# Kernel optimization log

Hardware: AMD Instinct MI355X
Metric: run time of the kernel (lower is better)

The kernel has to match this reference:

```python
import jax, jax.numpy as jnp
import numpy as np

B, K, N = 8192, 10, 100
LAM = 1.0


def _vec_transpose_P():
    # 9x9 vec-transpose permutation: P[3i+j, 3j+i] = 1 (the _getP matrix)
    P = np.zeros((9, 9), dtype=np.float32)
    for i in range(3):
        for j in range(3):
            P[3 * i + j, 3 * j + i] = 1.0
    return jnp.asarray(P)


def setup_inputs() -> dict:
    key = jax.random.key(0)
    k1, k2, k3 = jax.random.split(key, 3)
    weights = jax.random.uniform(k1, (N, 1), dtype=jnp.float32) + 0.1  # positive weights
    model_keypoints = jax.random.normal(k2, (K, 3, N), dtype=jnp.float32)
    y = jax.random.normal(k3, (B, 3, N), dtype=jnp.float32)
    return {"y": y, "weights": weights, "model_keypoints": model_keypoints}


def _pace_forward(y, weights, model_keypoints):
    n = model_keypoints.shape[-1]
    k = model_keypoints.shape[0]
    bsz = y.shape[0]
    w = weights                                  # (N,1)
    wsum = w.sum()
    b = model_keypoints                          # (K,3,N)
    b_w = (b @ w) / wsum                         # (K,3,1)
    sw = jnp.sqrt(w[:, 0])                       # (N,)

    # ---- precomputed constants (original __init__) ----
    bar_b = sw[None, None, :] * (b - b_w)                    # (K,3,N)
    bar_B = bar_b.transpose(0, 2, 1).reshape(k, 3 * n).T     # (3N,K), row idx 3n+a
    bar_H = 2.0 * (bar_B.T @ bar_B + LAM * jnp.eye(k, dtype=y.dtype))
    Hinv = jnp.linalg.inv(bar_H)
    Ht = Hinv @ jnp.ones((k, 1), dtype=y.dtype)
    denom = Ht.sum()
    G = Hinv - (Ht @ Ht.T) / denom               # (K,K)
    g = Ht / denom                               # (K,1)
    GBt = G @ bar_B.T                            # (K,3N)
    M = jnp.concatenate([2.0 * bar_B @ GBt - jnp.eye(3 * n, dtype=y.dtype),
                         2.0 * jnp.sqrt(LAM) * GBt], axis=0)       # (3N+K,3N)
    h = jnp.concatenate([bar_B @ g, jnp.sqrt(LAM) * g], axis=0)    # (3N+K,1)
    P = _vec_transpose_P().astype(y.dtype)

    # ---- forward ----
    y_w = (y @ w) / wsum                         # (B,3,1)
    bar_y = sw[None, None, :] * (y - y_w)        # (B,3,N)

    # E_b = M @ kron(Ybar_b^T, I3) @ P, done batched without materializing kron:
    # (M @ kron(Y^T, I3))[m, 3j+a] = sum_n M[m, 3n+a] * Y[j, n]
    Mr = M.reshape(-1, n, 3)                                  # Mr[m, nn, a] = M[m, 3nn+a]
    MB = jnp.einsum('mna,bjn->bmja', Mr, bar_y)               # (B,3N+K,3,3)
    E = MB.reshape(bsz, -1, 9) @ P                            # (B,3N+K,9)
    q00 = h[:, 0] @ h[:, 0]                                   # scalar h^T h
    hE = jnp.einsum('m,bmc->bc', h[:, 0], E)                  # (B,9)
    Q11 = jnp.einsum('bmc,bmd->bcd', E, E)                    # (B,9,9)
    top = jnp.concatenate([jnp.broadcast_to(q00, (bsz, 1, 1)), hE[:, None, :]], axis=2)
    bot = jnp.concatenate([hE[:, :, None], Q11], axis=2)
    Q = jnp.concatenate([top, bot], axis=1)                   # (B,10,10)

    # SDP relaxation: at a tight optimum X = v v^T with v the minimizer of v^T Q v,
    # recovered here as the eigenvector of Q with smallest eigenvalue (batched eigh)
    _, evec = jnp.linalg.eigh(Q)
    v = evec[:, :, 0]                                         # (B,10), ascending order
    v = v / v[:, :1]                                          # homogenize: v[0] = 1
    R = v[:, 1:].reshape(bsz, 3, 3).transpose(0, 2, 1)        # (B,3,3)

    # shape coefficients: c = 2 * G B^T * kron(I_N, R^T) vec(bar_y) + g
    RTy = jnp.einsum('bra,brn->bna', R, bar_y).reshape(bsz, 3 * n)   # idx 3n+a
    c = 2.0 * jnp.einsum('km,bm->bk', GBt, RTy)[:, :, None] + g[None, :, :]  # (B,K,1)
    # translation: t = y_w - R b_w^T c
    t = y_w - R @ jnp.einsum('ka,bko->bao', b_w[:, :, 0], c)  # (B,3,1)
    return R, t, c


def reference(y, weights, model_keypoints):
    return _pace_forward(y, weights, model_keypoints)
```

## Files before the change

kernel.cpp:

```cpp
#include <hip/hip_runtime.h>
#include <math.h>

#define LT_CT 0
#define LT_WT 3200
#define LT_SM 3304
#define LT_AR 3600
#define LT_TOT 11184

#define SM_WSUM 0
#define SM_RWS  1
#define SM_Q00  2
#define SM_Z2   4
#define SM_BS   16
#define SM_W    48
#define SM_G    148
#define SM_GV   248
#define SM_BW   260

#define A_YS 0
#define A_SF 4864
#define A_QL 6416
#define A_AX 7328

__host__ __device__ constexpr int TRI(int p,int q){ return p*10-(p*(p+1))/2+q; }
__host__ __device__ constexpr int SIDX(int a,int b){ return (a<=b)?TRI(a,b):TRI(b,a); }
__host__ __device__ constexpr int LTRI(int i,int j){ return i*(i+1)/2+j; }

template<int CTRL>
__device__ __forceinline__ float dpp_add(float v){
  int s = __builtin_amdgcn_mov_dpp(__float_as_int(v), CTRL, 0xF, 0xF, true);
  return v + __int_as_float(s);
}
__device__ __forceinline__ float gsum16(float v){
  v = dpp_add<0xB1>(v);
  v = dpp_add<0x4E>(v);
  v = dpp_add<0x141>(v);
  v = dpp_add<0x140>(v);
  return v;
}

__global__ __launch_bounds__(256,2) void pace_fused(const float* __restrict__ y,
                                                    const float* __restrict__ w,
                                                    const float* __restrict__ mk,
                                                    float* __restrict__ out){
  __shared__ __attribute__((aligned(16))) float S[LT_TOT];
  const int tid  = threadIdx.x;
  const int lane = tid & 63;
  const int sub  = tid & 15;
  const int item = tid >> 4;

  {
    float* s_mb = S+LT_AR;
    float* s_w  = S+LT_AR+3000;
    float* s_sw = S+LT_AR+3104;
    float* s_bw = S+LT_AR+3208;
    float* s_C  = S+LT_AR+3240;
    float* s_Hi = S+LT_AR+3340;
    float* s_G  = S+LT_AR+3440;
    float* s_T  = S+LT_AR+3540;
    float* s_gv = S+LT_AR+3640;
    float* s_Ht = S+LT_AR+3652;
    float* s_z  = S+LT_AR+3664;
    float* sm   = S+LT_SM;

    for (int i=tid;i<3000;i+=256) s_mb[i]=mk[i];
    for (int i=tid;i<100;i+=256){ float x=w[i]; s_w[i]=x; s_sw[i]=sqrtf(x); }
    __syncthreads();

    float av = s_w[lane] + ((lane<36)? s_w[lane+64] : 0.f);
    #pragma unroll
    for (int m=32;m;m>>=1) av += __shfl_xor(av,m);
    const float wsum = av;
    const float rws  = 1.0f/av;

    if (tid<30){
      const float4* p=(const float4*)&s_mb[tid*100];
      const float4* q=(const float4*)&s_w[0];
      float acc=0;
      #pragma unroll 5
      for (int j=0;j<25;j++){ float4 x=p[j], yv=q[j];
        acc=fmaf(x.x,yv.x,acc); acc=fmaf(x.y,yv.y,acc);
        acc=fmaf(x.z,yv.z,acc); acc=fmaf(x.w,yv.w,acc); }
      s_bw[tid]=acc*rws;
    }
    __syncthreads();
    for (int i=tid;i<3000;i+=256){ int r=i/100, n=i-r*100; s_mb[i]=s_sw[n]*(s_mb[i]-s_bw[r]); }
    __syncthreads();
    if (tid<100){
      int k=tid/10, k2=tid-10*(tid/10);
      const float4* p1=(const float4*)&s_mb[k*300];
      const float4* p2=(const float4*)&s_mb[k2*300];
      float acc=0;
      #pragma unroll 5
      for (int j=0;j<75;j++){ float4 x=p1[j], yv=p2[j];
        acc=fmaf(x.x,yv.x,acc); acc=fmaf(x.y,yv.y,acc);
        acc=fmaf(x.z,yv.z,acc); acc=fmaf(x.w,yv.w,acc); }
      s_C[tid]=acc;
    }
    __syncthreads();
    if (tid<64){
      float R[20];
      {
        int row=(tid<10)? tid : 0;
        #pragma unroll
        for (int c=0;c<10;c++) R[c]=2.0f*(s_C[row*10+c]+(c==row?1.0f:0.0f));
        #pragma unroll
        for (int c=0;c<10;c++) R[10+c]=(c==row)?1.0f:0.0f;
      }
      #pragma unroll
      for (int p=0;p<10;p++){
        float appv=__shfl(R[p],p);
        float ra=1.0f/appv;
        float fr=R[p];
        #pragma unroll
        for (int c=0;c<20;c++){
          float pc=__shfl(R[c],p)*ra;
          R[c]=(tid==p)? pc : fmaf(-fr,pc,R[c]);
        }
      }
      if (tid<10){
        float ht=0.f;
        #pragma unroll
        for (int c=0;c<10;c++){ s_Hi[tid*10+c]=R[10+c]; ht+=R[10+c]; }
        s_Ht[tid]=ht;
      }
    }
    __syncthreads();
    float dsum=0.f;
    #pragma unroll
    for (int k=0;k<10;k++) dsum+=s_Ht[k];
    const float rden=1.0f/dsum;
    if (tid<10) s_gv[tid]=s_Ht[tid]*rden;
    __syncthreads();
    if (tid<100){ int r=tid/10,c=tid-10*(tid/10); s_G[tid]=s_Hi[tid]-s_Ht[r]*s_Ht[c]*rden; }
    __syncthreads();
    if (tid<100){
      int r=tid/10,c=tid-10*(tid/10); float acc=0;
      #pragma unroll
      for (int j=0;j<10;j++) acc+=(s_C[r*10+j]+(r==j?1.0f:0.0f))*s_G[j*10+c];
      s_T[tid]=acc;
    }
    __syncthreads();
    if (tid<100){
      int r=tid/10,c=tid-10*(tid/10); float acc=0;
      #pragma unroll
      for (int j=0;j<10;j++) acc+=s_G[r*10+j]*s_T[j*10+c];
      sm[SM_W+tid]=4.0f*acc-4.0f*s_G[tid];
      sm[SM_G+tid]=s_G[tid];
    }
    if (tid<10){
      float acc=0;
      #pragma unroll
      for (int j=0;j<10;j++) acc+=(s_C[tid*10+j]+(tid==j?1.0f:0.0f))*s_gv[j];
      s_z[tid]=acc;
    }
    __syncthreads();
    if (tid<10){
      float acc=0;
      #pragma unroll
      for (int j=0;j<10;j++) acc+=s_G[tid*10+j]*s_z[j];
      sm[SM_Z2+tid]=2.0f*acc-s_gv[tid];
    }
    if (tid==0){
      float acc=0;
      #pragma unroll
      for (int r=0;r<10;r++){
        float rr=0;
        #pragma unroll
        for (int c=0;c<10;c++) rr+=s_C[r*10+c]*s_gv[c];
        acc+=s_gv[r]*rr+s_gv[r]*s_gv[r];
      }
      sm[SM_WSUM]=wsum; sm[SM_RWS]=rws; sm[SM_Q00]=acc; sm[3]=0.f;
    }
    for (int i=tid;i<3000;i+=256){
      int l=i/100, n=i-100*l;
      S[LT_CT + ((n>>2)*32 + l)*4 + (n&3)] = s_mb[i]*s_sw[n];
    }
    for (int i=tid;i<200;i+=256){ int c=i>>3, r=i&7; S[LT_CT+(c*32+30)*4+r]=0.f; }
    for (int i=tid;i<100;i+=256) S[LT_WT+i]=s_w[i];
    if (tid<30){
      const float4* p=(const float4*)&s_mb[tid*100];
      const float4* q=(const float4*)&s_sw[0];
      float acc=0;
      #pragma unroll 5
      for (int j=0;j<25;j++){ float4 x=p[j], yv=q[j];
        acc=fmaf(x.x,yv.x,acc); acc=fmaf(x.y,yv.y,acc);
        acc=fmaf(x.z,yv.z,acc); acc=fmaf(x.w,yv.w,acc); }
      sm[SM_BS+tid]=acc;
    }
    if (tid<2)  sm[SM_BS+30+tid]=0.f;
    if (tid<10) sm[SM_GV+tid]=s_gv[tid];
    if (tid<30) sm[SM_BW+tid]=s_bw[tid];
    __syncthreads();
  }

  const float* sm = S+LT_SM;
  float* yS = S+LT_AR+A_YS;
  float* sF = S+LT_AR+A_SF;
  float* sQ = S+LT_AR+A_QL;
  float* sX = S+LT_AR+A_AX;

  {
    const float4* yg = (const float4*)(y + (size_t)blockIdx.x*4800);
    #pragma unroll
    for (int r=0;r<5;r++){
      int f = tid + 256*r;
      if (f<1200){
        int it2=f/75, rem=f-75*it2;
        ((float4*)&yS[it2*304])[rem] = yg[f];
      }
    }
  }
  __syncthreads();

  const float* yb = &yS[item*304];

  float swy0=0,swy1=0,swy2=0,s00=0,s01=0,s02=0,s11=0,s12=0,s22=0;
  #pragma unroll
  for (int m=0;m<6;m++){
    int n=sub+16*m;
    float y0=yb[n], y1=yb[100+n], y2=yb[200+n];
    float wn=S[LT_WT+n];
    float wy0=wn*y0,wy1=wn*y1,wy2=wn*y2;
    swy0+=wy0;swy1+=wy1;swy2+=wy2;
    s00+=wy0*y0;s01+=wy0*y1;s02+=wy0*y2;s11+=wy1*y1;s12+=wy1*y2;s22+=wy2*y2;
  }
  if (sub<4){
    int n=96+sub;
    float y0=yb[n], y1=yb[100+n], y2=yb[200+n];
    float wn=S[LT_WT+n];
    float wy0=wn*y0,wy1=wn*y1,wy2=wn*y2;
    swy0+=wy0;swy1+=wy1;swy2+=wy2;
    s00+=wy0*y0;s01+=wy0*y1;s02+=wy0*y2;s11+=wy1*y1;s12+=wy1*y2;s22+=wy2*y2;
  }
  swy0=gsum16(swy0); swy1=gsum16(swy1); swy2=gsum16(swy2);
  s00=gsum16(s00); s01=gsum16(s01); s02=gsum16(s02);
  s11=gsum16(s11); s12=gsum16(s12); s22=gsum16(s22);

  const float wsum=sm[SM_WSUM], rws=sm[SM_RWS];
  const float yw0=swy0*rws, yw1=swy1*rws, yw2=swy2*rws;

  {
    float a0=0,a1=0,a2=0,b0=0,b1=0,b2=0;
    #pragma unroll 5
    for (int c=0;c<25;c++){
      float4 cfA = *(const float4*)&S[LT_CT+(c*32+sub)*4];
      float4 cfB = *(const float4*)&S[LT_CT+(c*32+sub+16)*4];
      float4 ya  = *(const float4*)&yb[4*c];
      float4 yB  = *(const float4*)&yb[100+4*c];
      float4 yc  = *(const float4*)&yb[200+4*c];
      a0=fmaf(cfA.x,ya.x,a0); a0=fmaf(cfA.y,ya.y,a0); a0=fmaf(cfA.z,ya.z,a0); a0=fmaf(cfA.w,ya.w,a0);
      a1=fmaf(cfA.x,yB.x,a1); a1=fmaf(cfA.y,yB.y,a1); a1=fmaf(cfA.z,yB.z,a1); a1=fmaf(cfA.w,yB.w,a1);
      a2=fmaf(cfA.x,yc.x,a2); a2=fmaf(cfA.y,yc.y,a2); a2=fmaf(cfA.z,yc.z,a2); a2=fmaf(cfA.w,yc.w,a2);
      b0=fmaf(cfB.x,ya.x,b0); b0=fmaf(cfB.y,ya.y,b0); b0=fmaf(cfB.z,ya.z,b0); b0=fmaf(cfB.w,ya.w,b0);
      b1=fmaf(cfB.x,yB.x,b1); b1=fmaf(cfB.y,yB.y,b1); b1=fmaf(cfB.z,yB.z,b1); b1=fmaf(cfB.w,yB.w,b1);
      b2=fmaf(cfB.x,yc.x,b2); b2=fmaf(cfB.y,yc.y,b2); b2=fmaf(cfB.z,yc.z,b2); b2=fmaf(cfB.w,yc.w,b2);
    }
    float bsA=sm[SM_BS+sub], bsB=sm[SM_BS+sub+16];
    a0-=yw0*bsA; a1-=yw1*bsA; a2-=yw2*bsA;
    b0-=yw0*bsB; b1-=yw1*bsB; b2-=yw2*bsB;
    sF[item*97+sub*3+0]=a0; sF[item*97+sub*3+1]=a1; sF[item*97+sub*3+2]=a2;
    sF[item*97+48+sub*3+0]=b0; sF[item*97+48+sub*3+1]=b1; sF[item*97+48+sub*3+2]=b2;
    if (sub==0){
      float* ax=&sX[item*16];
      ax[0]=yw0; ax[1]=yw1; ax[2]=yw2;
      ax[3+0]=s00-wsum*yw0*yw0;
      ax[3+4]=s11-wsum*yw1*yw1;
      ax[3+8]=s22-wsum*yw2*yw2;
      float g01=s01-wsum*yw0*yw1, g02=s02-wsum*yw0*yw2, g12=s12-wsum*yw1*yw2;
      ax[3+1]=g01; ax[3+3]=g01;
      ax[3+2]=g02; ax[3+6]=g02;
      ax[3+5]=g12; ax[3+7]=g12;
    }
  }
  __syncthreads();

  if (tid<144){
    int it2=tid/9, mp=tid-9*(tid/9);
    float fcol[10], t2[10];
    #pragma unroll
    for (int k=0;k<10;k++) fcol[k]=sF[it2*97+k*9+mp];
    #pragma unroll
    for (int k=0;k<10;k++){
      float acc=0;
      #pragma unroll
      for (int k2=0;k2<10;k2++) acc+=sm[SM_W+k*10+k2]*fcol[k2];
      t2[k]=acc;
    }
    float he=0;
    #pragma unroll
    for (int k=0;k<10;k++) he+=sm[SM_Z2+k]*fcol[k];
    sQ[it2*57 + 1+mp]=he;
    #pragma unroll 1
    for (int m=0;m<=mp;m++){
      float gd=sX[it2*16+3+(m%3)*3+(mp%3)];
      float acc=((m/3)==(mp/3))? gd : 0.f;
      #pragma unroll
      for (int k=0;k<10;k++) acc+=sF[it2*97+k*9+m]*t2[k];
      int p=1+m, q=1+mp;
      sQ[it2*57 + p*10-((p*(p+1))>>1)+q]=acc;
    }
  }
  if (tid>=144 && tid<160) sQ[(tid-144)*57]=sm[SM_Q00];
  __syncthreads();

  if (tid<16){
    const int it2=tid;
    const int gb2=blockIdx.x*16+it2;
    float A[55];
    #pragma unroll
    for (int e=0;e<55;e++) A[e]=sQ[it2*57+e];
    float dd[10], ee[9];
    #pragma unroll
    for (int k=0;k<8;k++){
      float nrm2=0.f;
      #pragma unroll
      for (int i=1;i<10;i++){ if (i<k+1) continue; float xi=A[SIDX(i,k)]; nrm2=fmaf(xi,xi,nrm2); }
      float x0=A[SIDX(k+1,k)];
      float nr=sqrtf(nrm2);
      float alpha=-copysignf(nr,x0);
      bool ok=nrm2>1e-30f;
      float v1=x0-alpha;
      float vtv=-2.0f*alpha*v1;
      float bh=ok?2.0f*__builtin_amdgcn_rcpf(vtv):0.f;
      ee[k]=ok?alpha:x0;
      float vv[10];
      #pragma unroll
      for (int i=0;i<10;i++) vv[i]=(i<k+1)?0.f:((i==k+1)?v1:A[SIDX(i,k)]);
      float p[10];
      #pragma unroll
      for (int i=0;i<10;i++){
        if (i<k+1){ p[i]=0.f; continue; }
        float acc=0;
        #pragma unroll
        for (int j=1;j<10;j++){ if (j<k+1) continue; acc+=A[SIDX(i,j)]*vv[j]; }
        p[i]=bh*acc;
      }
      float Kc=0.f;
      #pragma unroll
      for (int i=1;i<10;i++){ if (i<k+1) continue; Kc=fmaf(vv[i],p[i],Kc); }
      Kc*=0.5f*bh;
      float wv[10];
      #pragma unroll
      for (int i=0;i<10;i++) wv[i]=p[i]-Kc*vv[i];
      #pragma unroll
      for (int i=1;i<10;i++){
        if (i<k+1) continue;
        #pragma unroll
        for (int j=1;j<10;j++){
          if (j<i) continue;
          A[TRI(i,j)]-=vv[i]*wv[j]+wv[i]*vv[j];
        }
      }
    }
    ee[8]=A[TRI(8,9)];
    #pragma unroll
    for (int i=0;i<10;i++) dd[i]=A[TRI(i,i)];
    float esq[9];
    #pragma unroll
    for (int i=0;i<9;i++) esq[i]=ee[i]*ee[i];

    float scaleT=0.f, lo=1e30f, hi=1e30f;
    #pragma unroll
    for (int i=0;i<10;i++){
      float r=((i>0)?fabsf(ee[i-1]):0.f)+((i<9)?fabsf(ee[i]):0.f);
      scaleT=fmaxf(scaleT,fabsf(dd[i])+r);
      lo=fminf(lo,dd[i]-r);
      hi=fminf(hi,dd[i]);
    }
    hi+=1e-6f*scaleT+1e-30f;
    const float pm=1e-12f*scaleT+1e-37f;
    #pragma unroll 1
    for (int it=0;it<16;++it){
      float mid=0.5f*(lo+hi);
      float q=dd[0]-mid;
      q=(fabsf(q)<pm)?((q<0.f)?-pm:pm):q;
      int cnt=(q<0.f);
      #pragma unroll
      for (int i=1;i<10;i++){
        q=dd[i]-mid-esq[i-1]*__builtin_amdgcn_rcpf(q);
        q=(fabsf(q)<pm)?((q<0.f)?-pm:pm):q;
        cnt+=(q<0.f);
      }
      bool any=cnt>0;
      hi=any?mid:hi;
      lo=any?lo:mid;
    }
    const float sigma=lo-1e-5f*scaleT-1e-30f;
    const float pmL=1e-8f*scaleT+1e-37f;

    float Lc[55], rd[10];
    #pragma unroll
    for (int i=0;i<10;i++){
      #pragma unroll
      for (int j=0;j<10;j++){
        if (j>i) continue;
        float a=sQ[it2*57+SIDX(j,i)]-((i==j)?sigma:0.f);
        #pragma unroll
        for (int t2=0;t2<9;t2++){
          if (t2>=j) continue;
          a-=Lc[LTRI(i,t2)]*Lc[LTRI(j,t2)];
        }
        if (j<i) Lc[LTRI(i,j)]=a*rd[j];
        else { a=fmaxf(a,pmL); rd[i]=rsqrtf(a); Lc[LTRI(i,i)]=a*rd[i]; }
      }
    }
    float xv[10];
    #pragma unroll
    for (int i=0;i<10;i++) xv[i]=1.f;
    #pragma unroll 1
    for (int itr=0;itr<3;++itr){
      #pragma unroll
      for (int i=0;i<10;i++){
        float acc=xv[i];
        #pragma unroll
        for (int j=0;j<9;j++){ if (j>=i) continue; acc-=Lc[LTRI(i,j)]*xv[j]; }
        acc*=rd[i];
        xv[i]=fminf(fmaxf(acc,-1e15f),1e15f);
      }
      #pragma unroll
      for (int i=9;i>=0;i--){
        float acc=xv[i];
        #pragma unroll
        for (int j=9;j>0;j--){ if (j<=i) continue; acc-=Lc[LTRI(j,i)]*xv[j]; }
        acc*=rd[i];
        xv[i]=fminf(fmaxf(acc,-1e15f),1e15f);
      }
      float nn=0.f;
      #pragma unroll
      for (int i=0;i<10;i++) nn=fmaf(xv[i],xv[i],nn);
      nn=fmaxf(nn,1e-30f);
      float sc2=rsqrtf(nn);
      #pragma unroll
      for (int i=0;i<10;i++) xv[i]*=sc2;
    }
    float r0=1.0f/xv[0];
    float vn[10];
    vn[0]=1.f;
    #pragma unroll
    for (int m=1;m<10;m++) vn[m]=xv[m]*r0;

    float dv[10];
    #pragma unroll
    for (int k=0;k<10;k++){
      float acc=0;
      #pragma unroll
      for (int m=0;m<9;m++) acc+=vn[1+m]*sF[it2*97+k*9+m];
      dv[k]=acc;
    }
    float cv[10];
    #pragma unroll
    for (int k=0;k<10;k++){
      float acc=0;
      #pragma unroll
      for (int k2=0;k2<10;k2++) acc+=sm[SM_G+k*10+k2]*dv[k2];
      cv[k]=2.0f*acc+sm[SM_GV+k];
    }
    float e0=0,e1=0,e2=0;
    #pragma unroll
    for (int k=0;k<10;k++){
      e0+=sm[SM_BW+k*3+0]*cv[k];
      e1+=sm[SM_BW+k*3+1]*cv[k];
      e2+=sm[SM_BW+k*3+2]*cv[k];
    }
    float ywa=sX[it2*16+0], ywb=sX[it2*16+1], ywc=sX[it2*16+2];
    #pragma unroll
    for (int i=0;i<3;i++)
      #pragma unroll
      for (int j=0;j<3;j++)
        out[gb2*9+i*3+j]=vn[1+3*j+i];
    out[73728+gb2*3+0]=ywa-(vn[1]*e0+vn[4]*e1+vn[7]*e2);
    out[73728+gb2*3+1]=ywb-(vn[2]*e0+vn[5]*e1+vn[8]*e2);
    out[73728+gb2*3+2]=ywc-(vn[3]*e0+vn[6]*e1+vn[9]*e2);
    #pragma unroll
    for (int k=0;k<10;k++)
      out[98304+gb2*10+k]=cv[k];
  }
}

extern "C" void kernel_launch(void* const* d_in, const int* in_sizes, int n_in,
                              void* d_out, int out_size, void* d_ws, size_t ws_size,
                              hipStream_t stream) {
  const float* y  = (const float*)d_in[0];
  const float* w  = (const float*)d_in[1];
  const float* mk = (const float*)d_in[2];
  float* out = (float*)d_out;
  pace_fused<<<512, 256, 0, stream>>>(y, w, mk, out);
}
```

Baseline: 101.2 us.

## Halve items per block, use 32 lanes per item, double grid size

Each block now handles 8 batch items instead of 16, and 32 threads cooperate per item instead of 16. Each thread now computes one projection column group, where before it computed two. Reductions extend to 32 lanes with an extra ds_swizzle step. The smaller shared-memory footprint allows launch bounds of 4 blocks per CU, and the grid doubles to 1024 blocks. In exchange, every block still recomputes the full per-block constant setup (the K×K inverse and related precomputation), so that redundant prologue work doubles, and fewer threads are active in the eigen stage per block.

After: 112.8 us. 1.12x slower.

```diff
diff --git a/kernel.cpp b/kernel.cpp
--- a/kernel.cpp
+++ b/kernel.cpp
@@ -5,7 +5,7 @@
 #define LT_WT 3200
 #define LT_SM 3304
 #define LT_AR 3600
-#define LT_TOT 11184
+#define LT_TOT 7392
 
 #define SM_WSUM 0
 #define SM_RWS  1
@@ -18,9 +18,9 @@
 #define SM_BW   260
 
 #define A_YS 0
-#define A_SF 4864
-#define A_QL 6416
-#define A_AX 7328
+#define A_SF 2432
+#define A_QL 3208
+#define A_AX 3664
 
 __host__ __device__ constexpr int TRI(int p,int q){ return p*10-(p*(p+1))/2+q; }
 __host__ __device__ constexpr int SIDX(int a,int b){ return (a<=b)?TRI(a,b):TRI(b,a); }
@@ -31,23 +31,24 @@
   int s = __builtin_amdgcn_mov_dpp(__float_as_int(v), CTRL, 0xF, 0xF, true);
   return v + __int_as_float(s);
 }
-__device__ __forceinline__ float gsum16(float v){
+__device__ __forceinline__ float gsum32(float v){
   v = dpp_add<0xB1>(v);
   v = dpp_add<0x4E>(v);
   v = dpp_add<0x141>(v);
   v = dpp_add<0x140>(v);
+  v += __int_as_float(__builtin_amdgcn_ds_swizzle(__float_as_int(v), 0x401F));
   return v;
 }
 
-__global__ __launch_bounds__(256,2) void pace_fused(const float* __restrict__ y,
+__global__ __launch_bounds__(256,4) void pace_fused(const float* __restrict__ y,
                                                     const float* __restrict__ w,
                                                     const float* __restrict__ mk,
                                                     float* __restrict__ out){
   __shared__ __attribute__((aligned(16))) float S[LT_TOT];
   const int tid  = threadIdx.x;
   const int lane = tid & 63;
-  const int sub  = tid & 15;
-  const int item = tid >> 4;
+  const int sub  = tid & 31;
+  const int item = tid >> 5;
 
   {
     float* s_mb = S+LT_AR;
@@ -201,11 +202,11 @@
   float* sX = S+LT_AR+A_AX;
 
   {
-    const float4* yg = (const float4*)(y + (size_t)blockIdx.x*4800);
-    #pragma unroll
-    for (int r=0;r<5;r++){
+    const float4* yg = (const float4*)(y + (size_t)blockIdx.x*2400);
+    #pragma unroll
+    for (int r=0;r<3;r++){
       int f = tid + 256*r;
-      if (f<1200){
+      if (f<600){
         int it2=f/75, rem=f-75*it2;
         ((float4*)&yS[it2*304])[rem] = yg[f];
       }
@@ -217,8 +218,8 @@
 
   float swy0=0,swy1=0,swy2=0,s00=0,s01=0,s02=0,s11=0,s12=0,s22=0;
   #pragma unroll
-  for (int m=0;m<6;m++){
-    int n=sub+16*m;
+  for (int m=0;m<3;m++){
+    int n=sub+32*m;
     float y0=yb[n], y1=yb[100+n], y2=yb[200+n];
     float wn=S[LT_WT+n];
     float wy0=wn*y0,wy1=wn*y1,wy2=wn*y2;
@@ -233,34 +234,30 @@
     swy0+=wy0;swy1+=wy1;swy2+=wy2;
     s00+=wy0*y0;s01+=wy0*y1;s02+=wy0*y2;s11+=wy1*y1;s12+=wy1*y2;s22+=wy2*y2;
   }
-  swy0=gsum16(swy0); swy1=gsum16(swy1); swy2=gsum16(swy2);
-  s00=gsum16(s00); s01=gsum16(s01); s02=gsum16(s02);
-  s11=gsum16(s11); s12=gsum16(s12); s22=gsum16(s22);
+  swy0=gsum32(swy0); swy1=gsum32(swy1); swy2=gsum32(swy2);
+  s00=gsum32(s00); s01=gsum32(s01); s02=gsum32(s02);
+  s11=gsum32(s11); s12=gsum32(s12); s22=gsum32(s22);
 
   const float wsum=sm[SM_WSUM], rws=sm[SM_RWS];
   const float yw0=swy0*rws, yw1=swy1*rws, yw2=swy2*rws;
 
   {
-    float a0=0,a1=0,a2=0,b0=0,b1=0,b2=0;
+    float a0=0,a1=0,a2=0;
     #pragma unroll 5
     for (int c=0;c<25;c++){
-      float4 cfA = *(const float4*)&S[LT_CT+(c*32+sub)*4];
-      float4 cfB = *(const float4*)&S[LT_CT+(c*32+sub+16)*4];
-      float4 ya  = *(const float4*)&yb[4*c];
-      float4 yB  = *(const float4*)&yb[100+4*c];
-      float4 yc  = *(const float4*)&yb[200+4*c];
-      a0=fmaf(cfA.x,ya.x,a0); a0=fmaf(cfA.y,ya.y,a0); a0=fmaf(cfA.z,ya.z,a0); a0=fmaf(cfA.w,ya.w,a0);
-      a1=fmaf(cfA.x,yB.x,a1); a1=fmaf(cfA.y,yB.y,a1); a1=fmaf(cfA.z,yB.z,a1); a1=fmaf(cfA.w,yB.w,a1);
-      a2=fmaf(cfA.x,yc.x,a2); a2=fmaf(cfA.y,yc.y,a2); a2=fmaf(cfA.z,yc.z,a2); a2=fmaf(cfA.w,yc.w,a2);
-      b0=fmaf(cfB.x,ya.x,b0); b0=fmaf(cfB.y,ya.y,b0); b0=fmaf(cfB.z,ya.z,b0); b0=fmaf(cfB.w,ya.w,b0);
-      b1=fmaf(cfB.x,yB.x,b1); b1=fmaf(cfB.y,yB.y,b1); b1=fmaf(cfB.z,yB.z,b1); b1=fmaf(cfB.w,yB.w,b1);
-      b2=fmaf(cfB.x,yc.x,b2); b2=fmaf(cfB.y,yc.y,b2); b2=fmaf(cfB.z,yc.z,b2); b2=fmaf(cfB.w,yc.w,b2);
-    }
-    float bsA=sm[SM_BS+sub], bsB=sm[SM_BS+sub+16];
-    a0-=yw0*bsA; a1-=yw1*bsA; a2-=yw2*bsA;
-    b0-=yw0*bsB; b1-=yw1*bsB; b2-=yw2*bsB;
-    sF[item*97+sub*3+0]=a0; sF[item*97+sub*3+1]=a1; sF[item*97+sub*3+2]=a2;
-    sF[item*97+48+sub*3+0]=b0; sF[item*97+48+sub*3+1]=b1; sF[item*97+48+sub*3+2]=b2;
+      float4 cf = *(const float4*)&S[LT_CT+(c*32+sub)*4];
+      float4 ya = *(const float4*)&yb[4*c];
+      float4 yB = *(const float4*)&yb[100+4*c];
+      float4 yc = *(const float4*)&yb[200+4*c];
+      a0=fmaf(cf.x,ya.x,a0); a0=fmaf(cf.y,ya.y,a0); a0=fmaf(cf.z,ya.z,a0); a0=fmaf(cf.w,ya.w,a0);
+      a1=fmaf(cf.x,yB.x,a1); a1=fmaf(cf.y,yB.y,a1); a1=fmaf(cf.z,yB.z,a1); a1=fmaf(cf.w,yB.w,a1);
+      a2=fmaf(cf.x,yc.x,a2); a2=fmaf(cf.y,yc.y,a2); a2=fmaf(cf.z,yc.z,a2); a2=fmaf(cf.w,yc.w,a2);
+    }
+    if (sub<30){
+      float bsv=sm[SM_BS+sub];
+      a0-=yw0*bsv; a1-=yw1*bsv; a2-=yw2*bsv;
+      sF[item*97+sub*3+0]=a0; sF[item*97+sub*3+1]=a1; sF[item*97+sub*3+2]=a2;
+    }
     if (sub==0){
       float* ax=&sX[item*16];
       ax[0]=yw0; ax[1]=yw1; ax[2]=yw2;
@@ -275,7 +272,7 @@
   }
   __syncthreads();
 
-  if (tid<144){
+  if (tid<72){
     int it2=tid/9, mp=tid-9*(tid/9);
     float fcol[10], t2[10];
     #pragma unroll
@@ -301,12 +298,12 @@
       sQ[it2*57 + p*10-((p*(p+1))>>1)+q]=acc;
     }
   }
-  if (tid>=144 && tid<160) sQ[(tid-144)*57]=sm[SM_Q00];
+  if (tid>=72 && tid<80) sQ[(tid-72)*57]=sm[SM_Q00];
   __syncthreads();
 
-  if (tid<16){
+  if (tid<8){
     const int it2=tid;
-    const int gb2=blockIdx.x*16+it2;
+    const int gb2=blockIdx.x*8+it2;
     float A[55];
     #pragma unroll
     for (int e=0;e<55;e++) A[e]=sQ[it2*57+e];
@@ -485,5 +482,5 @@
   const float* w  = (const float*)d_in[1];
   const float* mk = (const float*)d_in[2];
   float* out = (float*)d_out;
-  pace_fused<<<512, 256, 0, stream>>>(y, w, mk, out);
+  pace_fused<<<1024, 256, 0, stream>>>(y, w, mk, out);
 }
```

## Fold centering and sqrt-weight scaling algebraically into per-block setup

Applied to the files above, without the earlier changes.

Each block's constant setup stops building explicitly centered, sqrt-weighted keypoints. The Gram matrix C now comes from raw weighted moments minus an outer-product correction, and the per-item correction uses b_w times the weighted y sums. This drops two barriers, the centering pass, the sqrt computations and one extra dot-product pass. The cost is a slightly different floating-point summation order in the subtraction form, which can lose some precision.

Measured after the change: 99.91 us. Within noise of the previous version (-1.2%).

```diff
diff --git a/kernel.cpp b/kernel.cpp
--- a/kernel.cpp
+++ b/kernel.cpp
@@ -11,7 +11,6 @@
 #define SM_RWS  1
 #define SM_Q00  2
 #define SM_Z2   4
-#define SM_BS   16
 #define SM_W    48
 #define SM_G    148
 #define SM_GV   248
@@ -52,19 +51,18 @@
   {
     float* s_mb = S+LT_AR;
     float* s_w  = S+LT_AR+3000;
-    float* s_sw = S+LT_AR+3104;
-    float* s_bw = S+LT_AR+3208;
-    float* s_C  = S+LT_AR+3240;
-    float* s_Hi = S+LT_AR+3340;
-    float* s_G  = S+LT_AR+3440;
-    float* s_T  = S+LT_AR+3540;
-    float* s_gv = S+LT_AR+3640;
-    float* s_Ht = S+LT_AR+3652;
-    float* s_z  = S+LT_AR+3664;
+    float* s_M1 = S+LT_AR+3104;
+    float* s_C  = S+LT_AR+3136;
+    float* s_Hi = S+LT_AR+3236;
+    float* s_G  = S+LT_AR+3336;
+    float* s_T  = S+LT_AR+3436;
+    float* s_gv = S+LT_AR+3536;
+    float* s_Ht = S+LT_AR+3548;
+    float* s_z  = S+LT_AR+3560;
     float* sm   = S+LT_SM;
 
     for (int i=tid;i<3000;i+=256) s_mb[i]=mk[i];
-    for (int i=tid;i<100;i+=256){ float x=w[i]; s_w[i]=x; s_sw[i]=sqrtf(x); }
+    for (int i=tid;i<100;i+=256){ float x=w[i]; s_w[i]=x; S[LT_WT+i]=x; }
     __syncthreads();
 
     float av = s_w[lane] + ((lane<36)? s_w[lane+64] : 0.f);
@@ -73,6 +71,11 @@
     const float wsum = av;
     const float rws  = 1.0f/av;
 
+    for (int i=tid;i<3000;i+=256){
+      int l=i/100, n=i-100*l;
+      S[LT_CT + ((n>>2)*32 + l)*4 + (n&3)] = s_w[n]*s_mb[i];
+    }
+    for (int i=tid;i<200;i+=256){ int c=i>>3, r=i&7; S[LT_CT+(c*32+30)*4+r]=0.f; }
     if (tid<30){
       const float4* p=(const float4*)&s_mb[tid*100];
       const float4* q=(const float4*)&s_w[0];
@@ -81,23 +84,33 @@
       for (int j=0;j<25;j++){ float4 x=p[j], yv=q[j];
         acc=fmaf(x.x,yv.x,acc); acc=fmaf(x.y,yv.y,acc);
         acc=fmaf(x.z,yv.z,acc); acc=fmaf(x.w,yv.w,acc); }
-      s_bw[tid]=acc*rws;
-    }
-    __syncthreads();
-    for (int i=tid;i<3000;i+=256){ int r=i/100, n=i-r*100; s_mb[i]=s_sw[n]*(s_mb[i]-s_bw[r]); }
-    __syncthreads();
+      s_M1[tid]=acc;
+    }
+    __syncthreads();
+
     if (tid<100){
       int k=tid/10, k2=tid-10*(tid/10);
-      const float4* p1=(const float4*)&s_mb[k*300];
-      const float4* p2=(const float4*)&s_mb[k2*300];
-      float acc=0;
-      #pragma unroll 5
-      for (int j=0;j<75;j++){ float4 x=p1[j], yv=p2[j];
-        acc=fmaf(x.x,yv.x,acc); acc=fmaf(x.y,yv.y,acc);
-        acc=fmaf(x.z,yv.z,acc); acc=fmaf(x.w,yv.w,acc); }
+      float acc=0;
+      #pragma unroll
+      for (int j=0;j<3;j++){
+        int la=3*k+j, lb=3*k2+j;
+        const float4* p2=(const float4*)&s_mb[lb*100];
+        float part=0;
+        #pragma unroll 5
+        for (int c=0;c<25;c++){
+          float4 a=*(const float4*)&S[LT_CT+(c*32+la)*4];
+          float4 b=p2[c];
+          part=fmaf(a.x,b.x,part); part=fmaf(a.y,b.y,part);
+          part=fmaf(a.z,b.z,part); part=fmaf(a.w,b.w,part);
+        }
+        acc += part - s_M1[la]*s_M1[lb]*rws;
+      }
       s_C[tid]=acc;
     }
-    __syncthreads();
+    if (tid>=128 && tid<158) sm[SM_BW+(tid-128)] = s_M1[tid-128]*rws;
+    if (tid>=158 && tid<160) sm[SM_BW+30+(tid-158)] = 0.f;
+    __syncthreads();
+
     if (tid<64){
       float R[20];
       {
@@ -172,25 +185,7 @@
       }
       sm[SM_WSUM]=wsum; sm[SM_RWS]=rws; sm[SM_Q00]=acc; sm[3]=0.f;
     }
-    for (int i=tid;i<3000;i+=256){
-      int l=i/100, n=i-100*l;
-      S[LT_CT + ((n>>2)*32 + l)*4 + (n&3)] = s_mb[i]*s_sw[n];
-    }
-    for (int i=tid;i<200;i+=256){ int c=i>>3, r=i&7; S[LT_CT+(c*32+30)*4+r]=0.f; }
-    for (int i=tid;i<100;i+=256) S[LT_WT+i]=s_w[i];
-    if (tid<30){
-      const float4* p=(const float4*)&s_mb[tid*100];
-      const float4* q=(const float4*)&s_sw[0];
-      float acc=0;
-      #pragma unroll 5
-      for (int j=0;j<25;j++){ float4 x=p[j], yv=q[j];
-        acc=fmaf(x.x,yv.x,acc); acc=fmaf(x.y,yv.y,acc);
-        acc=fmaf(x.z,yv.z,acc); acc=fmaf(x.w,yv.w,acc); }
-      sm[SM_BS+tid]=acc;
-    }
-    if (tid<2)  sm[SM_BS+30+tid]=0.f;
     if (tid<10) sm[SM_GV+tid]=s_gv[tid];
-    if (tid<30) sm[SM_BW+tid]=s_bw[tid];
     __syncthreads();
   }
 
@@ -256,9 +251,9 @@
       b1=fmaf(cfB.x,yB.x,b1); b1=fmaf(cfB.y,yB.y,b1); b1=fmaf(cfB.z,yB.z,b1); b1=fmaf(cfB.w,yB.w,b1);
       b2=fmaf(cfB.x,yc.x,b2); b2=fmaf(cfB.y,yc.y,b2); b2=fmaf(cfB.z,yc.z,b2); b2=fmaf(cfB.w,yc.w,b2);
     }
-    float bsA=sm[SM_BS+sub], bsB=sm[SM_BS+sub+16];
-    a0-=yw0*bsA; a1-=yw1*bsA; a2-=yw2*bsA;
-    b0-=yw0*bsB; b1-=yw1*bsB; b2-=yw2*bsB;
+    float bwA=sm[SM_BW+sub], bwB=sm[SM_BW+sub+16];
+    a0-=bwA*swy0; a1-=bwA*swy1; a2-=bwA*swy2;
+    b0-=bwB*swy0; b1-=bwB*swy1; b2-=bwB*swy2;
     sF[item*97+sub*3+0]=a0; sF[item*97+sub*3+1]=a1; sF[item*97+sub*3+2]=a2;
     sF[item*97+48+sub*3+0]=b0; sF[item*97+48+sub*3+1]=b1; sF[item*97+48+sub*3+2]=b2;
     if (sub==0){
```
